# Optimization experiments

Measured on AMD Instinct MI355X. Metric: run time of the kernel, lower is better.

## Reference

```python
import jax, jax.numpy as jnp
import numpy as np

N_USERS = 50000
N_ITEMS = 100000
N_NODES = N_USERS + N_ITEMS
N_EDGES = 2000000
EMBED = 64
N_LAYERS = 3
BATCH = 8192
NEG_SLOPE = 0.01  # torch LeakyReLU default
EPS = 1e-12       # torch F.normalize default


def setup_inputs() -> dict:
    key = jax.random.key(0)
    ks = jax.random.split(key, 12)
    return {
        "user_emb": jax.random.normal(ks[0], (N_USERS, EMBED), jnp.float32) * 0.1,
        "item_emb": jax.random.normal(ks[1], (N_ITEMS, EMBED), jnp.float32) * 0.1,
        "W1": jax.random.normal(ks[2], (N_LAYERS, EMBED, EMBED), jnp.float32) * 0.1,
        "b1": jax.random.normal(ks[3], (N_LAYERS, EMBED), jnp.float32) * 0.01,
        "W2": jax.random.normal(ks[4], (N_LAYERS, EMBED, EMBED), jnp.float32) * 0.1,
        "b2": jax.random.normal(ks[5], (N_LAYERS, EMBED), jnp.float32) * 0.01,
        "adj_vals": jax.random.uniform(ks[6], (N_EDGES,), jnp.float32),
        "adj_rows": jax.random.randint(ks[7], (N_EDGES,), 0, N_NODES, jnp.int32),
        "adj_cols": jax.random.randint(ks[8], (N_EDGES,), 0, N_NODES, jnp.int32),
        "u": jax.random.randint(ks[9], (BATCH,), 0, N_USERS, jnp.int32),
        "i": jax.random.randint(ks[10], (BATCH,), 0, N_ITEMS, jnp.int32),
        "j": jax.random.randint(ks[11], (BATCH,), 0, N_ITEMS, jnp.int32),
    }


def _spmm(rows, cols, vals, x):
    # sparse [N,N] @ dense [N,d] via gather + segment-sum
    return jax.ops.segment_sum(vals[:, None] * x[cols], rows, num_segments=N_NODES)


def _forward(user_emb, item_emb, W1, b1, W2, b2, adj_vals, adj_rows, adj_cols, u, i, j):
    emb = jnp.concatenate([user_emb, item_emb], axis=0)  # [N, d]
    finals = [emb]
    for l in range(N_LAYERS):
        t1e = _spmm(adj_rows, adj_cols, adj_vals, emb)        # A @ E
        t1 = t1e @ W1[l].T + b1[l]                             # Linear W1
        t2 = (emb * t1e) @ W2[l].T + b2[l]                     # Linear W2 on E (.) AE
        emb = jax.nn.leaky_relu(t1 + t2, NEG_SLOPE)
        norm = jnp.sqrt(jnp.sum(emb * emb, axis=1, keepdims=True))
        finals.append(emb / jnp.maximum(norm, EPS))
    fin = jnp.concatenate(finals, axis=1)                      # [N, d*(L+1)]
    fin_u, fin_i = fin[:N_USERS], fin[N_USERS:]
    bu, bp, bn = fin_u[u], fin_i[i], fin_i[j]
    pos_y = jnp.sum(bu * bp, axis=1)
    neg_y = jnp.sum(bu * bn, axis=1)
    return -jnp.mean(jax.nn.log_sigmoid(pos_y - neg_y))


def reference(user_emb, item_emb, W1, b1, W2, b2, adj_vals, adj_rows, adj_cols, u, i, j):
    return _forward(user_emb, item_emb, W1, b1, W2, b2, adj_vals, adj_rows, adj_cols, u, i, j)
```

## Files before the change

kernel.cpp:

```cpp
#include <hip/hip_runtime.h>
#include <hip/hip_bf16.h>
#include <math.h>

#define N_USERS 50000
#define N_ITEMS 100000
#define N_NODES 150000
#define N_EDGES 2000000
#define EMBED 64
#define N_LAYERS 3
#define BATCH 8192
#define BATCH3 (3 * BATCH)

#define BSHIFT 9
#define BROWS 512
#define NBKT ((N_NODES + BROWS - 1) / BROWS)
#define EPB 4096

typedef __bf16 bf16x8 __attribute__((ext_vector_type(8)));
typedef float  f32x4  __attribute__((ext_vector_type(4)));

__device__ __forceinline__ float bf2f(unsigned short u) {
    union { unsigned int i; float f; } c; c.i = ((unsigned int)u) << 16; return c.f;
}
__device__ __forceinline__ unsigned short f2bf(float f) {
    __hip_bfloat16 h = __float2bfloat16(f);
    union { __hip_bfloat16 h; unsigned short u; } c; c.h = h; return c.u;
}
__device__ __forceinline__ bf16x8 as_bf8(uint4 u) {
    union { uint4 u; bf16x8 v; } c; c.u = u; return c.v;
}
__device__ __forceinline__ void unpack8(uint4 u, float* f) {
    union { unsigned int i; float x; } c;
    c.i = u.x << 16; f[0] = c.x; c.i = u.x & 0xffff0000u; f[1] = c.x;
    c.i = u.y << 16; f[2] = c.x; c.i = u.y & 0xffff0000u; f[3] = c.x;
    c.i = u.z << 16; f[4] = c.x; c.i = u.z & 0xffff0000u; f[5] = c.x;
    c.i = u.w << 16; f[6] = c.x; c.i = u.w & 0xffff0000u; f[7] = c.x;
}
__device__ __forceinline__ bf16x8 pack8(const float* f) {
    union { unsigned short s[8]; bf16x8 v; } u;
#pragma unroll
    for (int j = 0; j < 8; j++) u.s[j] = f2bf(f[j]);
    return u.v;
}
__device__ __forceinline__ void gacc(uint4 w, float v, float* acc) {
    union { unsigned int i; float f; } cv;
    cv.i = w.x << 16;          acc[0] += v * cv.f;
    cv.i = w.x & 0xffff0000u;  acc[1] += v * cv.f;
    cv.i = w.y << 16;          acc[2] += v * cv.f;
    cv.i = w.y & 0xffff0000u;  acc[3] += v * cv.f;
    cv.i = w.z << 16;          acc[4] += v * cv.f;
    cv.i = w.z & 0xffff0000u;  acc[5] += v * cv.f;
    cv.i = w.w << 16;          acc[6] += v * cv.f;
    cv.i = w.w & 0xffff0000u;  acc[7] += v * cv.f;
}

__global__ __launch_bounds__(256) void k_tobf16(const float4* __restrict__ ue,
                                                const float4* __restrict__ ie,
                                                ushort4* __restrict__ tab) {
    int idx = blockIdx.x * 256 + threadIdx.x;
    const int TOT = N_NODES * EMBED / 4;
    const int UPART = N_USERS * EMBED / 4;
    if (idx < TOT) {
        float4 v = (idx < UPART) ? ue[idx] : ie[idx - UPART];
        ushort4 o;
        o.x = f2bf(v.x); o.y = f2bf(v.y); o.z = f2bf(v.z); o.w = f2bf(v.w);
        tab[idx] = o;
    }
}

__global__ __launch_bounds__(256) void k_wprep(const float* __restrict__ W1,
                                               const float* __restrict__ b1,
                                               const float* __restrict__ W2,
                                               const float* __restrict__ b2,
                                               unsigned short* __restrict__ Wb,
                                               float* __restrict__ bsum) {
    int idx = blockIdx.x * 256 + threadIdx.x;
    if (idx < 3 * 64 * 128) {
        int l = idx >> 13, rem = idx & 8191;
        int n = rem >> 7, k = rem & 127;
        float w = (k < 64) ? W1[l * 4096 + n * 64 + k] : W2[l * 4096 + n * 64 + (k - 64)];
        Wb[idx] = f2bf(w);
    } else if (idx < 3 * 64 * 128 + 192) {
        int t = idx - 3 * 64 * 128;
        bsum[t] = b1[t] + b2[t];
    }
}

__global__ __launch_bounds__(256) void k_bkt_count(const int* __restrict__ rows,
                                                   int* __restrict__ bkt_count) {
    __shared__ int hist[NBKT];
    int tid = threadIdx.x;
    for (int t = tid; t < NBKT; t += 256) hist[t] = 0;
    __syncthreads();
    int e = (blockIdx.x * 256 + tid) * 4;
    if (e + 3 < N_EDGES) {
        int4 r = *(const int4*)&rows[e];
        atomicAdd(&hist[r.x >> BSHIFT], 1);
        atomicAdd(&hist[r.y >> BSHIFT], 1);
        atomicAdd(&hist[r.z >> BSHIFT], 1);
        atomicAdd(&hist[r.w >> BSHIFT], 1);
    } else {
        for (int k = 0; k < 4; k++)
            if (e + k < N_EDGES) atomicAdd(&hist[rows[e + k] >> BSHIFT], 1);
    }
    __syncthreads();
    for (int t = tid; t < NBKT; t += 256)
        if (hist[t] > 0) atomicAdd(&bkt_count[t], hist[t]);
}

__global__ __launch_bounds__(512) void k_bkt_scan(const int* __restrict__ bkt_count,
                                                  int* __restrict__ bkt_base,
                                                  int* __restrict__ bkt_cursor,
                                                  int* __restrict__ row_ptr) {
    int tid = threadIdx.x;
    int x = (tid < NBKT) ? bkt_count[tid] : 0;
    int lane = tid & 63, wid = tid >> 6;
    int v = x;
    for (int o = 1; o < 64; o <<= 1) {
        int t = __shfl_up(v, o);
        if (lane >= o) v += t;
    }
    __shared__ int wsum[8];
    if (lane == 63) wsum[wid] = v;
    __syncthreads();
    int add = 0;
    for (int w = 0; w < wid; w++) add += wsum[w];
    int incl = add + v;
    int excl = incl - x;
    if (tid < NBKT) {
        bkt_base[tid]   = excl;
        bkt_cursor[tid] = excl;
    }
    if (tid == NBKT - 1) {
        bkt_base[NBKT]    = incl;
        row_ptr[N_NODES]  = incl;
    }
}

__global__ __launch_bounds__(256) void k_bucketA(const int* __restrict__ rows,
                                                 const int* __restrict__ cols,
                                                 const float* __restrict__ vals,
                                                 int* __restrict__ bkt_cursor,
                                                 int4* __restrict__ bucketed) {
    __shared__ int sr[EPB];
    __shared__ int sc[EPB];
    __shared__ int sv[EPB];
    __shared__ int hist[NBKT];
    __shared__ int cbase[NBKT];
    int tid = threadIdx.x;
    int e0 = blockIdx.x * EPB;
    int cnt = N_EDGES - e0; if (cnt > EPB) cnt = EPB;

    for (int i = tid; i < cnt; i += 256) {
        sr[i] = rows[e0 + i];
        sc[i] = cols[e0 + i];
        sv[i] = __float_as_int(vals[e0 + i]);
    }
    for (int t = tid; t < NBKT; t += 256) hist[t] = 0;
    __syncthreads();
    for (int i = tid; i < cnt; i += 256) atomicAdd(&hist[sr[i] >> BSHIFT], 1);
    __syncthreads();
    for (int t = tid; t < NBKT; t += 256)
        cbase[t] = (hist[t] > 0) ? atomicAdd(&bkt_cursor[t], hist[t]) : 0;
    __syncthreads();
    for (int t = tid; t < NBKT; t += 256) hist[t] = 0;
    __syncthreads();
    for (int i = tid; i < cnt; i += 256) {
        int b = sr[i] >> BSHIFT;
        int off = atomicAdd(&hist[b], 1);
        bucketed[cbase[b] + off] = make_int4(sr[i], sc[i], sv[i], 0);
    }
}

__global__ __launch_bounds__(1024) void k_bucketC(const int* __restrict__ bkt_base,
                                                  const int4* __restrict__ bucketed,
                                                  int* __restrict__ row_ptr,
                                                  int2* __restrict__ edges) {
    __shared__ int hist[BROWS];
    __shared__ int ssum[BROWS];
    __shared__ int cur[BROWS];
    int b = blockIdx.x, tid = threadIdx.x;
    int base = bkt_base[b];
    int cnt  = bkt_base[b + 1] - base;
    int row0 = b << BSHIFT;

    if (tid < BROWS) hist[tid] = 0;
    __syncthreads();
    for (int i = tid; i < cnt; i += 1024)
        atomicAdd(&hist[bucketed[base + i].x - row0], 1);
    __syncthreads();
    int own = 0;
    if (tid < BROWS) { own = hist[tid]; ssum[tid] = own; }
    __syncthreads();
    for (int off = 1; off < BROWS; off <<= 1) {
        int t = 0;
        if (tid < BROWS && tid >= off) t = ssum[tid - off];
        __syncthreads();
        if (tid < BROWS) ssum[tid] += t;
        __syncthreads();
    }
    if (tid < BROWS) {
        int excl = ssum[tid] - own;
        int grow = row0 + tid;
        if (grow < N_NODES) row_ptr[grow] = base + excl;
        cur[tid] = excl;
    }
    __syncthreads();
    for (int i = tid; i < cnt; i += 1024) {
        int4 ed = bucketed[base + i];
        int lr  = ed.x - row0;
        int off = atomicAdd(&cur[lr], 1);
        edges[base + off] = make_int2(ed.y, ed.z);
    }
}

__global__ __launch_bounds__(256) void k_spmm(const int*  __restrict__ row_ptr,
                                              const int2* __restrict__ edges,
                                              const unsigned short* __restrict__ tab,
                                              unsigned short* __restrict__ t1eH) {
    int wave = threadIdx.x >> 6, lane = threadIdx.x & 63;
    int row = blockIdx.x * 4 + wave;
    int slot = lane >> 3;
    int sl   = lane & 7;
    int s = row_ptr[row], e = row_ptr[row + 1];
    float acc[8] = {};
    int p = s + slot;
    for (; p + 8 < e; p += 16) {
        int2 ed0 = edges[p];
        int2 ed1 = edges[p + 8];
        uint4 w0 = *(const uint4*)&tab[ed0.x * EMBED + 8 * sl];
        uint4 w1 = *(const uint4*)&tab[ed1.x * EMBED + 8 * sl];
        gacc(w0, __int_as_float(ed0.y), acc);
        gacc(w1, __int_as_float(ed1.y), acc);
    }
    if (p < e) {
        int2 ed = edges[p];
        uint4 w = *(const uint4*)&tab[ed.x * EMBED + 8 * sl];
        gacc(w, __int_as_float(ed.y), acc);
    }
#pragma unroll
    for (int k = 0; k < 8; k++) {
        acc[k] += __shfl_xor(acc[k], 8);
        acc[k] += __shfl_xor(acc[k], 16);
        acc[k] += __shfl_xor(acc[k], 32);
    }
    if (slot == 0) {
        uint4 o;
        o.x = (unsigned)f2bf(acc[0]) | ((unsigned)f2bf(acc[1]) << 16);
        o.y = (unsigned)f2bf(acc[2]) | ((unsigned)f2bf(acc[3]) << 16);
        o.z = (unsigned)f2bf(acc[4]) | ((unsigned)f2bf(acc[5]) << 16);
        o.w = (unsigned)f2bf(acc[6]) | ((unsigned)f2bf(acc[7]) << 16);
        *(uint4*)&t1eH[row * EMBED + 8 * sl] = o;
    }
}

__device__ __forceinline__ int map_row(int bb, const int* u, const int* ii, const int* jj) {
    if (bb < BATCH) return u[bb];
    if (bb < 2 * BATCH) return N_USERS + ii[bb - BATCH];
    return N_USERS + jj[bb - 2 * BATCH];
}

__global__ __launch_bounds__(256) void k_spmm_t(const int*  __restrict__ row_ptr,
                                                const int2* __restrict__ edges,
                                                const unsigned short* __restrict__ tab,
                                                unsigned short* __restrict__ t1eS,
                                                const int* __restrict__ u,
                                                const int* __restrict__ ii,
                                                const int* __restrict__ jj) {
    int wave = threadIdx.x >> 6, lane = threadIdx.x & 63;
    int bb = blockIdx.x * 4 + wave;
    int row = map_row(bb, u, ii, jj);
    int slot = lane >> 3, sl = lane & 7;
    int s = row_ptr[row], e = row_ptr[row + 1];
    float acc[8] = {};
    int p = s + slot;
    for (; p + 8 < e; p += 16) {
        int2 ed0 = edges[p];
        int2 ed1 = edges[p + 8];
        uint4 w0 = *(const uint4*)&tab[ed0.x * EMBED + 8 * sl];
        uint4 w1 = *(const uint4*)&tab[ed1.x * EMBED + 8 * sl];
        gacc(w0, __int_as_float(ed0.y), acc);
        gacc(w1, __int_as_float(ed1.y), acc);
    }
    if (p < e) {
        int2 ed = edges[p];
        uint4 w = *(const uint4*)&tab[ed.x * EMBED + 8 * sl];
        gacc(w, __int_as_float(ed.y), acc);
    }
#pragma unroll
    for (int k = 0; k < 8; k++) {
        acc[k] += __shfl_xor(acc[k], 8);
        acc[k] += __shfl_xor(acc[k], 16);
        acc[k] += __shfl_xor(acc[k], 32);
    }
    if (slot == 0) {
        uint4 o;
        o.x = (unsigned)f2bf(acc[0]) | ((unsigned)f2bf(acc[1]) << 16);
        o.y = (unsigned)f2bf(acc[2]) | ((unsigned)f2bf(acc[3]) << 16);
        o.z = (unsigned)f2bf(acc[4]) | ((unsigned)f2bf(acc[5]) << 16);
        o.w = (unsigned)f2bf(acc[6]) | ((unsigned)f2bf(acc[7]) << 16);
        *(uint4*)&t1eS[bb * EMBED + 8 * sl] = o;
    }
}

__global__ __launch_bounds__(256) void k_dense(const unsigned short* __restrict__ t1eH,
                                               const unsigned short* __restrict__ embH_in,
                                               unsigned short* __restrict__ embH_out,
                                               const unsigned short* __restrict__ Wb,
                                               const float* __restrict__ bsum) {
    int tid  = threadIdx.x;
    int wave = tid >> 6, lane = tid & 63;
    int r16  = lane & 15, hi = lane >> 4;
    int rowt0 = blockIdx.x * 64 + wave * 16;
    int row   = rowt0 + r16;
    bool ok   = row < N_NODES;

    uint4 z4 = make_uint4(0u, 0u, 0u, 0u);
    const unsigned short* trow = t1eH    + (size_t)row * EMBED;
    const unsigned short* erow = embH_in + (size_t)row * EMBED;
    uint4 t_lo = ok ? *(const uint4*)(trow + hi * 8)      : z4;
    uint4 t_hi = ok ? *(const uint4*)(trow + 32 + hi * 8) : z4;
    uint4 e_lo = ok ? *(const uint4*)(erow + hi * 8)      : z4;
    uint4 e_hi = ok ? *(const uint4*)(erow + 32 + hi * 8) : z4;

    bf16x8 A0 = as_bf8(t_lo);
    bf16x8 A1 = as_bf8(t_hi);
    float ta[8], ea[8], pa[8];
    unpack8(t_lo, ta); unpack8(e_lo, ea);
#pragma unroll
    for (int j = 0; j < 8; j++) pa[j] = ta[j] * ea[j];
    bf16x8 A2 = pack8(pa);
    unpack8(t_hi, ta); unpack8(e_hi, ea);
#pragma unroll
    for (int j = 0; j < 8; j++) pa[j] = ta[j] * ea[j];
    bf16x8 A3 = pack8(pa);

#pragma unroll
    for (int nt = 0; nt < 4; nt++) {
        int wrow = nt * 16 + r16;
        const unsigned short* wp = Wb + wrow * 128 + hi * 8;
        bf16x8 B0 = as_bf8(*(const uint4*)(wp));
        bf16x8 B1 = as_bf8(*(const uint4*)(wp + 32));
        bf16x8 B2 = as_bf8(*(const uint4*)(wp + 64));
        bf16x8 B3 = as_bf8(*(const uint4*)(wp + 96));
        f32x4 c = {0.f, 0.f, 0.f, 0.f};
        c = __builtin_amdgcn_mfma_f32_16x16x32_bf16(A0, B0, c, 0, 0, 0);
        c = __builtin_amdgcn_mfma_f32_16x16x32_bf16(A1, B1, c, 0, 0, 0);
        c = __builtin_amdgcn_mfma_f32_16x16x32_bf16(A2, B2, c, 0, 0, 0);
        c = __builtin_amdgcn_mfma_f32_16x16x32_bf16(A3, B3, c, 0, 0, 0);

        int col = nt * 16 + r16;
        float bias = bsum[col];
#pragma unroll
        for (int r = 0; r < 4; r++) {
            int orow = rowt0 + hi * 4 + r;
            if (orow < N_NODES) {
                float v = c[r] + bias;
                v = (v > 0.f) ? v : 0.01f * v;
                embH_out[(size_t)orow * EMBED + col] = f2bf(v);
            }
        }
    }
}

__global__ __launch_bounds__(256) void k_dense_t(const unsigned short* __restrict__ t1eS,
                                                 const unsigned short* __restrict__ embH_in,
                                                 unsigned short* __restrict__ t2out,
                                                 const unsigned short* __restrict__ Wb,
                                                 const float* __restrict__ bsum,
                                                 const int* __restrict__ u,
                                                 const int* __restrict__ ii,
                                                 const int* __restrict__ jj) {
    int tid  = threadIdx.x;
    int wave = tid >> 6, lane = tid & 63;
    int r16  = lane & 15, hi = lane >> 4;
    int rowt0 = blockIdx.x * 64 + wave * 16;
    int bb   = rowt0 + r16;
    int nrow = map_row(bb, u, ii, jj);

    const unsigned short* trow = t1eS    + (size_t)bb   * EMBED;
    const unsigned short* erow = embH_in + (size_t)nrow * EMBED;
    uint4 t_lo = *(const uint4*)(trow + hi * 8);
    uint4 t_hi = *(const uint4*)(trow + 32 + hi * 8);
    uint4 e_lo = *(const uint4*)(erow + hi * 8);
    uint4 e_hi = *(const uint4*)(erow + 32 + hi * 8);

    bf16x8 A0 = as_bf8(t_lo);
    bf16x8 A1 = as_bf8(t_hi);
    float ta[8], ea[8], pa[8];
    unpack8(t_lo, ta); unpack8(e_lo, ea);
#pragma unroll
    for (int j = 0; j < 8; j++) pa[j] = ta[j] * ea[j];
    bf16x8 A2 = pack8(pa);
    unpack8(t_hi, ta); unpack8(e_hi, ea);
#pragma unroll
    for (int j = 0; j < 8; j++) pa[j] = ta[j] * ea[j];
    bf16x8 A3 = pack8(pa);

#pragma unroll
    for (int nt = 0; nt < 4; nt++) {
        int wrow = nt * 16 + r16;
        const unsigned short* wp = Wb + wrow * 128 + hi * 8;
        bf16x8 B0 = as_bf8(*(const uint4*)(wp));
        bf16x8 B1 = as_bf8(*(const uint4*)(wp + 32));
        bf16x8 B2 = as_bf8(*(const uint4*)(wp + 64));
        bf16x8 B3 = as_bf8(*(const uint4*)(wp + 96));
        f32x4 c = {0.f, 0.f, 0.f, 0.f};
        c = __builtin_amdgcn_mfma_f32_16x16x32_bf16(A0, B0, c, 0, 0, 0);
        c = __builtin_amdgcn_mfma_f32_16x16x32_bf16(A1, B1, c, 0, 0, 0);
        c = __builtin_amdgcn_mfma_f32_16x16x32_bf16(A2, B2, c, 0, 0, 0);
        c = __builtin_amdgcn_mfma_f32_16x16x32_bf16(A3, B3, c, 0, 0, 0);

        int col = nt * 16 + r16;
        float bias = bsum[col];
#pragma unroll
        for (int r = 0; r < 4; r++) {
            int obb = rowt0 + hi * 4 + r;
            float v = c[r] + bias;
            v = (v > 0.f) ? v : 0.01f * v;
            t2out[(size_t)obb * EMBED + col] = f2bf(v);
        }
    }
}

__global__ __launch_bounds__(256) void k_score0(const float* __restrict__ ue,
                                                const float* __restrict__ ie,
                                                const int* __restrict__ u,
                                                const int* __restrict__ ii,
                                                const int* __restrict__ jj,
                                                float* __restrict__ posAcc,
                                                float* __restrict__ negAcc) {
    int wave = threadIdx.x >> 6, lane = threadIdx.x & 63;
    int b = blockIdx.x * 4 + wave;
    float eu = ue[u[b]  * EMBED + lane];
    float ep = ie[ii[b] * EMBED + lane];
    float en = ie[jj[b] * EMBED + lane];
    float p = eu * ep, n = eu * en;
    for (int o = 1; o < 64; o <<= 1) {
        p += __shfl_xor(p, o);
        n += __shfl_xor(n, o);
    }
    if (lane == 0) {
        posAcc[b] += p;
        negAcc[b] += n;
    }
}

__global__ __launch_bounds__(256) void k_score1(const unsigned short* __restrict__ tab,
                                                const int* __restrict__ u,
                                                const int* __restrict__ ii,
                                                const int* __restrict__ jj,
                                                float* __restrict__ posAcc,
                                                float* __restrict__ negAcc) {
    int wave = threadIdx.x >> 6, lane = threadIdx.x & 63;
    int b = blockIdx.x * 4 + wave;
    int ru = u[b];
    int ri = N_USERS + ii[b];
    int rj = N_USERS + jj[b];
    float eu = bf2f(tab[ru * EMBED + lane]);
    float ep = bf2f(tab[ri * EMBED + lane]);
    float en = bf2f(tab[rj * EMBED + lane]);
    float su = eu * eu, sp = ep * ep, sn = en * en;
    for (int o = 1; o < 64; o <<= 1) {
        su += __shfl_xor(su, o);
        sp += __shfl_xor(sp, o);
        sn += __shfl_xor(sn, o);
    }
    eu /= fmaxf(sqrtf(su), 1e-12f);
    ep /= fmaxf(sqrtf(sp), 1e-12f);
    en /= fmaxf(sqrtf(sn), 1e-12f);
    float p = eu * ep, n = eu * en;
    for (int o = 1; o < 64; o <<= 1) {
        p += __shfl_xor(p, o);
        n += __shfl_xor(n, o);
    }
    if (lane == 0) {
        posAcc[b] += p;
        negAcc[b] += n;
    }
}

__global__ __launch_bounds__(256) void k_score1t(const unsigned short* __restrict__ t2out,
                                                 float* __restrict__ posAcc,
                                                 float* __restrict__ negAcc) {
    int wave = threadIdx.x >> 6, lane = threadIdx.x & 63;
    int b = blockIdx.x * 4 + wave;
    float eu = bf2f(t2out[(size_t)b * EMBED + lane]);
    float ep = bf2f(t2out[(size_t)(BATCH + b) * EMBED + lane]);
    float en = bf2f(t2out[(size_t)(2 * BATCH + b) * EMBED + lane]);
    float su = eu * eu, sp = ep * ep, sn = en * en;
    for (int o = 1; o < 64; o <<= 1) {
        su += __shfl_xor(su, o);
        sp += __shfl_xor(sp, o);
        sn += __shfl_xor(sn, o);
    }
    eu /= fmaxf(sqrtf(su), 1e-12f);
    ep /= fmaxf(sqrtf(sp), 1e-12f);
    en /= fmaxf(sqrtf(sn), 1e-12f);
    float p = eu * ep, n = eu * en;
    for (int o = 1; o < 64; o <<= 1) {
        p += __shfl_xor(p, o);
        n += __shfl_xor(n, o);
    }
    if (lane == 0) {
        posAcc[b] += p;
        negAcc[b] += n;
    }
}

__global__ __launch_bounds__(256) void k_loss(const float* __restrict__ pa,
                                              const float* __restrict__ na,
                                              float* __restrict__ out) {
    int b = blockIdx.x * 256 + threadIdx.x;
    float z = pa[b] - na[b];
    float x = -z;
    float sp = fmaxf(x, 0.f) + log1pf(expf(-fabsf(x)));
    for (int o = 1; o < 64; o <<= 1) sp += __shfl_xor(sp, o);
    __shared__ float s[4];
    int wave = threadIdx.x >> 6, lane = threadIdx.x & 63;
    if (lane == 0) s[wave] = sp;
    __syncthreads();
    if (threadIdx.x == 0) {
        float t = s[0] + s[1] + s[2] + s[3];
        atomicAdd(out, t * (1.f / (float)BATCH));
    }
}

extern "C" void kernel_launch(void* const* d_in, const int* in_sizes, int n_in,
                              void* d_out, int out_size, void* d_ws, size_t ws_size,
                              hipStream_t stream) {
    const float* user_emb = (const float*)d_in[0];
    const float* item_emb = (const float*)d_in[1];
    const float* W1       = (const float*)d_in[2];
    const float* b1       = (const float*)d_in[3];
    const float* W2       = (const float*)d_in[4];
    const float* b2       = (const float*)d_in[5];
    const float* adj_vals = (const float*)d_in[6];
    const int*   adj_rows = (const int*)d_in[7];
    const int*   adj_cols = (const int*)d_in[8];
    const int*   u_idx    = (const int*)d_in[9];
    const int*   i_idx    = (const int*)d_in[10];
    const int*   j_idx    = (const int*)d_in[11];
    float* out = (float*)d_out;

    char* ws = (char*)d_ws;
    unsigned short* t1eH       = (unsigned short*)(ws);
    unsigned short* t1eS       = (unsigned short*)(ws);
    unsigned short* t2out      = (unsigned short*)(ws + 4000000);
    int4*           bucketed   = (int4*)(ws);
    unsigned short* Wb         = (unsigned short*)(ws + 20000000);
    float*          bsum       = (float*)(ws + 20100000);
    int*            bkt_count  = (int*)(ws + 32000000);
    int*            bkt_base   = (int*)(ws + 32004096);
    int*            bkt_cursor = (int*)(ws + 32008192);
    unsigned short* HA         = (unsigned short*)(ws + 38400000);
    unsigned short* HB         = (unsigned short*)(ws + 57600000);
    int*            row_ptr    = (int*)(ws + 76800000);
    int2*           edges      = (int2*)(ws + 78000128);
    float*          posAcc     = (float*)(ws + 94000128);
    float*          negAcc     = (float*)(ws + 94032896);

    hipMemsetAsync(bkt_count, 0, 4096, stream);
    hipMemsetAsync(posAcc, 0, 2 * BATCH * sizeof(float), stream);
    hipMemsetAsync(d_out, 0, sizeof(float), stream);

    k_tobf16<<<(N_NODES * EMBED / 4 + 255) / 256, 256, 0, stream>>>(
        (const float4*)user_emb, (const float4*)item_emb, (ushort4*)HA);

    k_bkt_count<<<(N_EDGES / 4 + 255) / 256, 256, 0, stream>>>(adj_rows, bkt_count);
    k_bkt_scan<<<1, 512, 0, stream>>>(bkt_count, bkt_base, bkt_cursor, row_ptr);
    k_bucketA<<<(N_EDGES + EPB - 1) / EPB, 256, 0, stream>>>(adj_rows, adj_cols, adj_vals,
                                                             bkt_cursor, bucketed);
    k_bucketC<<<NBKT, 1024, 0, stream>>>(bkt_base, bucketed, row_ptr, edges);

    k_wprep<<<97, 256, 0, stream>>>(W1, b1, W2, b2, Wb, bsum);

    k_score0<<<BATCH / 4, 256, 0, stream>>>(user_emb, item_emb, u_idx, i_idx, j_idx,
                                            posAcc, negAcc);

    const int SGRID = N_NODES / 4;
    const int DGRID = (N_NODES + 63) / 64;

    k_spmm<<<SGRID, 256, 0, stream>>>(row_ptr, edges, HA, t1eH);
    k_dense<<<DGRID, 256, 0, stream>>>(t1eH, HA, HB, Wb, bsum);
    k_score1<<<BATCH / 4, 256, 0, stream>>>(HB, u_idx, i_idx, j_idx, posAcc, negAcc);

    k_spmm<<<SGRID, 256, 0, stream>>>(row_ptr, edges, HB, t1eH);
    k_dense<<<DGRID, 256, 0, stream>>>(t1eH, HB, HA, Wb + 8192, bsum + 64);
    k_score1<<<BATCH / 4, 256, 0, stream>>>(HA, u_idx, i_idx, j_idx, posAcc, negAcc);

    k_spmm_t<<<BATCH3 / 4, 256, 0, stream>>>(row_ptr, edges, HA, t1eS,
                                             u_idx, i_idx, j_idx);
    k_dense_t<<<BATCH3 / 64, 256, 0, stream>>>(t1eS, HA, t2out, Wb + 16384, bsum + 128,
                                               u_idx, i_idx, j_idx);
    k_score1t<<<BATCH / 4, 256, 0, stream>>>(t2out, posAcc, negAcc);

    k_loss<<<BATCH / 256, 256, 0, stream>>>(posAcc, negAcc, out);
}
```

Baseline: 342.8 us.

## Gather fp8 embedding copies in SpMM and pack bucketed edges into int2

Keeps an fp8 (e4m3) copy of each layer's node embeddings, written by the table-conversion kernel and by the dense kernel. The SpMM gathers now read this copy, half the bytes of bf16, and unpack it with hardware fp8-to-f32 conversions. Separately, the bucketing intermediate packs the local row and the column into one int instead of storing an int4, halving that scratch traffic. The fp8 gather adds quantization error to the aggregated neighbor sums, and the dense kernel does extra byte-wide stores.

```diff
diff --git a/kernel.cpp b/kernel.cpp
--- a/kernel.cpp
+++ b/kernel.cpp
@@ -26,6 +26,9 @@
     __hip_bfloat16 h = __float2bfloat16(f);
     union { __hip_bfloat16 h; unsigned short u; } c; c.h = h; return c.u;
 }
+__device__ __forceinline__ unsigned char f2q8(float x) {
+    return (unsigned char)(__builtin_amdgcn_cvt_pk_fp8_f32(x, x, 0, false) & 0xff);
+}
 __device__ __forceinline__ bf16x8 as_bf8(uint4 u) {
     union { uint4 u; bf16x8 v; } c; c.u = u; return c.v;
 }
@@ -42,21 +45,21 @@
     for (int j = 0; j < 8; j++) u.s[j] = f2bf(f[j]);
     return u.v;
 }
-__device__ __forceinline__ void gacc(uint4 w, float v, float* acc) {
-    union { unsigned int i; float f; } cv;
-    cv.i = w.x << 16;          acc[0] += v * cv.f;
-    cv.i = w.x & 0xffff0000u;  acc[1] += v * cv.f;
-    cv.i = w.y << 16;          acc[2] += v * cv.f;
-    cv.i = w.y & 0xffff0000u;  acc[3] += v * cv.f;
-    cv.i = w.z << 16;          acc[4] += v * cv.f;
-    cv.i = w.z & 0xffff0000u;  acc[5] += v * cv.f;
-    cv.i = w.w << 16;          acc[6] += v * cv.f;
-    cv.i = w.w & 0xffff0000u;  acc[7] += v * cv.f;
-}
-
-__global__ __launch_bounds__(256) void k_tobf16(const float4* __restrict__ ue,
-                                                const float4* __restrict__ ie,
-                                                ushort4* __restrict__ tab) {
+__device__ __forceinline__ void qacc(uint2 w, float v, float* acc) {
+    auto f0 = __builtin_amdgcn_cvt_pk_f32_fp8(w.x, false);
+    auto f1 = __builtin_amdgcn_cvt_pk_f32_fp8(w.x, true);
+    auto f2 = __builtin_amdgcn_cvt_pk_f32_fp8(w.y, false);
+    auto f3 = __builtin_amdgcn_cvt_pk_f32_fp8(w.y, true);
+    acc[0] += v * f0[0]; acc[1] += v * f0[1];
+    acc[2] += v * f1[0]; acc[3] += v * f1[1];
+    acc[4] += v * f2[0]; acc[5] += v * f2[1];
+    acc[6] += v * f3[0]; acc[7] += v * f3[1];
+}
+
+__global__ __launch_bounds__(256) void k_tabs(const float4* __restrict__ ue,
+                                              const float4* __restrict__ ie,
+                                              ushort4* __restrict__ tab,
+                                              unsigned int* __restrict__ q8) {
     int idx = blockIdx.x * 256 + threadIdx.x;
     const int TOT = N_NODES * EMBED / 4;
     const int UPART = N_USERS * EMBED / 4;
@@ -65,6 +68,9 @@
         ushort4 o;
         o.x = f2bf(v.x); o.y = f2bf(v.y); o.z = f2bf(v.z); o.w = f2bf(v.w);
         tab[idx] = o;
+        unsigned int lo = (unsigned int)__builtin_amdgcn_cvt_pk_fp8_f32(v.x, v.y, 0, false) & 0xffffu;
+        unsigned int hi = (unsigned int)__builtin_amdgcn_cvt_pk_fp8_f32(v.z, v.w, 0, false) & 0xffffu;
+        q8[idx] = lo | (hi << 16);
     }
 }
 
@@ -141,7 +147,7 @@
                                                  const int* __restrict__ cols,
                                                  const float* __restrict__ vals,
                                                  int* __restrict__ bkt_cursor,
-                                                 int4* __restrict__ bucketed) {
+                                                 int2* __restrict__ bucketed) {
     __shared__ int sr[EPB];
     __shared__ int sc[EPB];
     __shared__ int sv[EPB];
@@ -166,14 +172,16 @@
     for (int t = tid; t < NBKT; t += 256) hist[t] = 0;
     __syncthreads();
     for (int i = tid; i < cnt; i += 256) {
-        int b = sr[i] >> BSHIFT;
+        int r = sr[i];
+        int b = r >> BSHIFT;
+        int lr = r & (BROWS - 1);
         int off = atomicAdd(&hist[b], 1);
-        bucketed[cbase[b] + off] = make_int4(sr[i], sc[i], sv[i], 0);
+        bucketed[cbase[b] + off] = make_int2((lr << 18) | sc[i], sv[i]);
     }
 }
 
 __global__ __launch_bounds__(1024) void k_bucketC(const int* __restrict__ bkt_base,
-                                                  const int4* __restrict__ bucketed,
+                                                  const int2* __restrict__ bucketed,
                                                   int* __restrict__ row_ptr,
                                                   int2* __restrict__ edges) {
     __shared__ int hist[BROWS];
@@ -187,7 +195,7 @@
     if (tid < BROWS) hist[tid] = 0;
     __syncthreads();
     for (int i = tid; i < cnt; i += 1024)
-        atomicAdd(&hist[bucketed[base + i].x - row0], 1);
+        atomicAdd(&hist[bucketed[base + i].x >> 18], 1);
     __syncthreads();
     int own = 0;
     if (tid < BROWS) { own = hist[tid]; ssum[tid] = own; }
@@ -207,16 +215,16 @@
     }
     __syncthreads();
     for (int i = tid; i < cnt; i += 1024) {
-        int4 ed = bucketed[base + i];
-        int lr  = ed.x - row0;
+        int2 ed = bucketed[base + i];
+        int lr  = ed.x >> 18;
         int off = atomicAdd(&cur[lr], 1);
-        edges[base + off] = make_int2(ed.y, ed.z);
+        edges[base + off] = make_int2(ed.x & 0x3ffff, ed.y);
     }
 }
 
 __global__ __launch_bounds__(256) void k_spmm(const int*  __restrict__ row_ptr,
                                               const int2* __restrict__ edges,
-                                              const unsigned short* __restrict__ tab,
+                                              const unsigned char* __restrict__ q8,
                                               unsigned short* __restrict__ t1eH) {
     int wave = threadIdx.x >> 6, lane = threadIdx.x & 63;
     int row = blockIdx.x * 4 + wave;
@@ -228,15 +236,15 @@
     for (; p + 8 < e; p += 16) {
         int2 ed0 = edges[p];
         int2 ed1 = edges[p + 8];
-        uint4 w0 = *(const uint4*)&tab[ed0.x * EMBED + 8 * sl];
-        uint4 w1 = *(const uint4*)&tab[ed1.x * EMBED + 8 * sl];
-        gacc(w0, __int_as_float(ed0.y), acc);
-        gacc(w1, __int_as_float(ed1.y), acc);
+        uint2 w0 = *(const uint2*)&q8[ed0.x * EMBED + 8 * sl];
+        uint2 w1 = *(const uint2*)&q8[ed1.x * EMBED + 8 * sl];
+        qacc(w0, __int_as_float(ed0.y), acc);
+        qacc(w1, __int_as_float(ed1.y), acc);
     }
     if (p < e) {
         int2 ed = edges[p];
-        uint4 w = *(const uint4*)&tab[ed.x * EMBED + 8 * sl];
-        gacc(w, __int_as_float(ed.y), acc);
+        uint2 w = *(const uint2*)&q8[ed.x * EMBED + 8 * sl];
+        qacc(w, __int_as_float(ed.y), acc);
     }
 #pragma unroll
     for (int k = 0; k < 8; k++) {
@@ -262,7 +270,7 @@
 
 __global__ __launch_bounds__(256) void k_spmm_t(const int*  __restrict__ row_ptr,
                                                 const int2* __restrict__ edges,
-                                                const unsigned short* __restrict__ tab,
+                                                const unsigned char* __restrict__ q8,
                                                 unsigned short* __restrict__ t1eS,
                                                 const int* __restrict__ u,
                                                 const int* __restrict__ ii,
@@ -277,15 +285,15 @@
     for (; p + 8 < e; p += 16) {
         int2 ed0 = edges[p];
         int2 ed1 = edges[p + 8];
-        uint4 w0 = *(const uint4*)&tab[ed0.x * EMBED + 8 * sl];
-        uint4 w1 = *(const uint4*)&tab[ed1.x * EMBED + 8 * sl];
-        gacc(w0, __int_as_float(ed0.y), acc);
-        gacc(w1, __int_as_float(ed1.y), acc);
+        uint2 w0 = *(const uint2*)&q8[ed0.x * EMBED + 8 * sl];
+        uint2 w1 = *(const uint2*)&q8[ed1.x * EMBED + 8 * sl];
+        qacc(w0, __int_as_float(ed0.y), acc);
+        qacc(w1, __int_as_float(ed1.y), acc);
     }
     if (p < e) {
         int2 ed = edges[p];
-        uint4 w = *(const uint4*)&tab[ed.x * EMBED + 8 * sl];
-        gacc(w, __int_as_float(ed.y), acc);
+        uint2 w = *(const uint2*)&q8[ed.x * EMBED + 8 * sl];
+        qacc(w, __int_as_float(ed.y), acc);
     }
 #pragma unroll
     for (int k = 0; k < 8; k++) {
@@ -306,6 +314,7 @@
 __global__ __launch_bounds__(256) void k_dense(const unsigned short* __restrict__ t1eH,
                                                const unsigned short* __restrict__ embH_in,
                                                unsigned short* __restrict__ embH_out,
+                                               unsigned char* __restrict__ q8out,
                                                const unsigned short* __restrict__ Wb,
                                                const float* __restrict__ bsum) {
     int tid  = threadIdx.x;
@@ -358,6 +367,7 @@
                 float v = c[r] + bias;
                 v = (v > 0.f) ? v : 0.01f * v;
                 embH_out[(size_t)orow * EMBED + col] = f2bf(v);
+                q8out[(size_t)orow * EMBED + col]    = f2q8(v);
             }
         }
     }
@@ -547,9 +557,10 @@
     unsigned short* t1eH       = (unsigned short*)(ws);
     unsigned short* t1eS       = (unsigned short*)(ws);
     unsigned short* t2out      = (unsigned short*)(ws + 4000000);
-    int4*           bucketed   = (int4*)(ws);
+    int2*           bucketed   = (int2*)(ws);
     unsigned short* Wb         = (unsigned short*)(ws + 20000000);
     float*          bsum       = (float*)(ws + 20100000);
+    unsigned char*  Q8         = (unsigned char*)(ws + 20200000);
     int*            bkt_count  = (int*)(ws + 32000000);
     int*            bkt_base   = (int*)(ws + 32004096);
     int*            bkt_cursor = (int*)(ws + 32008192);
@@ -564,9 +575,6 @@
     hipMemsetAsync(posAcc, 0, 2 * BATCH * sizeof(float), stream);
     hipMemsetAsync(d_out, 0, sizeof(float), stream);
 
-    k_tobf16<<<(N_NODES * EMBED / 4 + 255) / 256, 256, 0, stream>>>(
-        (const float4*)user_emb, (const float4*)item_emb, (ushort4*)HA);
-
     k_bkt_count<<<(N_EDGES / 4 + 255) / 256, 256, 0, stream>>>(adj_rows, bkt_count);
     k_bkt_scan<<<1, 512, 0, stream>>>(bkt_count, bkt_base, bkt_cursor, row_ptr);
     k_bucketA<<<(N_EDGES + EPB - 1) / EPB, 256, 0, stream>>>(adj_rows, adj_cols, adj_vals,
@@ -574,6 +582,8 @@
     k_bucketC<<<NBKT, 1024, 0, stream>>>(bkt_base, bucketed, row_ptr, edges);
 
     k_wprep<<<97, 256, 0, stream>>>(W1, b1, W2, b2, Wb, bsum);
+    k_tabs<<<(N_NODES * EMBED / 4 + 255) / 256, 256, 0, stream>>>(
+        (const float4*)user_emb, (const float4*)item_emb, (ushort4*)HA, (unsigned int*)Q8);
 
     k_score0<<<BATCH / 4, 256, 0, stream>>>(user_emb, item_emb, u_idx, i_idx, j_idx,
                                             posAcc, negAcc);
@@ -581,15 +591,15 @@
     const int SGRID = N_NODES / 4;
     const int DGRID = (N_NODES + 63) / 64;
 
-    k_spmm<<<SGRID, 256, 0, stream>>>(row_ptr, edges, HA, t1eH);
-    k_dense<<<DGRID, 256, 0, stream>>>(t1eH, HA, HB, Wb, bsum);
+    k_spmm<<<SGRID, 256, 0, stream>>>(row_ptr, edges, Q8, t1eH);
+    k_dense<<<DGRID, 256, 0, stream>>>(t1eH, HA, HB, Q8, Wb, bsum);
     k_score1<<<BATCH / 4, 256, 0, stream>>>(HB, u_idx, i_idx, j_idx, posAcc, negAcc);
 
-    k_spmm<<<SGRID, 256, 0, stream>>>(row_ptr, edges, HB, t1eH);
-    k_dense<<<DGRID, 256, 0, stream>>>(t1eH, HB, HA, Wb + 8192, bsum + 64);
+    k_spmm<<<SGRID, 256, 0, stream>>>(row_ptr, edges, Q8, t1eH);
+    k_dense<<<DGRID, 256, 0, stream>>>(t1eH, HB, HA, Q8, Wb + 8192, bsum + 64);
     k_score1<<<BATCH / 4, 256, 0, stream>>>(HA, u_idx, i_idx, j_idx, posAcc, negAcc);
 
-    k_spmm_t<<<BATCH3 / 4, 256, 0, stream>>>(row_ptr, edges, HA, t1eS,
+    k_spmm_t<<<BATCH3 / 4, 256, 0, stream>>>(row_ptr, edges, Q8, t1eS,
                                              u_idx, i_idx, j_idx);
     k_dense_t<<<BATCH3 / 64, 256, 0, stream>>>(t1eS, HA, t2out, Wb + 16384, bsum + 128,
                                                u_idx, i_idx, j_idx);
```

Result: no change. 340.9 us (-0.5%).
